# Optimization experiments

Measured on AMD Instinct MI355X. Metric: run time of the kernel, lower is better.

## Reference

```python
import jax, jax.numpy as jnp
import numpy as np

NUM_FEAT = 10
C_IN = 64


def setup_inputs() -> dict:
    key = jax.random.key(0)
    ks = jax.random.split(key, 8)
    B, T, C, H, W = 1, 8, C_IN, 32, 32
    scale = 1.0 / np.sqrt(C)
    return {
        "input1": jax.random.normal(ks[0], (B, T, C, H, W), dtype=jnp.float32),
        "input2": jax.random.normal(ks[1], (B, T, C, H, W), dtype=jnp.float32),
        "w1": jax.random.normal(ks[2], (NUM_FEAT, C), dtype=jnp.float32) * scale,
        "b1": jax.random.normal(ks[3], (NUM_FEAT,), dtype=jnp.float32) * scale,
        "w2": jax.random.normal(ks[4], (NUM_FEAT, C), dtype=jnp.float32) * scale,
        "b2": jax.random.normal(ks[5], (NUM_FEAT,), dtype=jnp.float32) * scale,
        "w3": jax.random.normal(ks[6], (NUM_FEAT, C), dtype=jnp.float32) * scale,
        "b3": jax.random.normal(ks[7], (NUM_FEAT,), dtype=jnp.float32) * scale,
    }


def reference(input1, input2, w1, b1, w2, b2, w3, b3):
    B, T, C, H, W = input1.shape
    N = T * H * W
    # transpose(1,2).reshape -> [B, C, T*H*W]
    x1 = input1.transpose(0, 2, 1, 3, 4).reshape(B, C, N)
    x2 = input2.transpose(0, 2, 1, 3, 4).reshape(B, C, N)
    # 1x1 Conv1d projections (act == 0 -> ReLU branch)
    q = jnp.einsum('fc,bcn->bnf', w1, x1) + b1            # [B, N, F]
    k = jnp.einsum('fc,bcn->bfn', w2, x2) + b2[:, None]   # [B, F, N]
    v = jnp.einsum('fc,bcn->bnf', w3, x1) + b3            # [B, N, F]
    scores = jax.nn.relu(jnp.einsum('bnf,bfm->bnm', q, k))  # [B, N, N]
    out = jnp.einsum('bnm,bmf->bnf', scores, v)             # [B, N, F]
    # view([B,T,H,W,F]).permute(0,1,4,2,3)
    return out.reshape(B, T, H, W, -1).transpose(0, 1, 4, 2, 3)
```

## Files before the change

kernel.cpp:

```cpp
#include <hip/hip_runtime.h>

typedef short  sv8 __attribute__((ext_vector_type(8)));
typedef float  fv16 __attribute__((ext_vector_type(16)));
typedef unsigned int uv4 __attribute__((ext_vector_type(4)));
typedef unsigned int uint32;
typedef unsigned short ushort16;

#define NF      10
#define CIN     64
#define NTOT    8192
#define HW      1024
#define FPAD    16
#define MSPLIT  16
#define MCHUNK  (NTOT / MSPLIT)
#define PSTRIDE 16

#define MFMA32(a, b, c) __builtin_amdgcn_mfma_f32_32x32x16_bf16((a), (b), (c), 0, 0, 0)

static __device__ inline ushort16 f32_to_bf16_rne(float x) {
    uint32 u = __builtin_bit_cast(uint32, x);
    u = (u + 0x7fffu + ((u >> 16) & 1u)) >> 16;
    return (ushort16)u;
}

__global__ __launch_bounds__(64) void qkv_kernel(
    const float* __restrict__ in1, const float* __restrict__ in2,
    const float* __restrict__ w1, const float* __restrict__ b1,
    const float* __restrict__ w2, const float* __restrict__ b2,
    const float* __restrict__ w3, const float* __restrict__ b3,
    ushort16* __restrict__ qb, ushort16* __restrict__ kb,
    ushort16* __restrict__ vfrag)
{
    __shared__ ushort16 lvs[64][FPAD];

    const int tid = threadIdx.x;
    const int n  = blockIdx.x * 64 + tid;
    const int t  = n >> 10;
    const int hw = n & 1023;

    if (blockIdx.y == 0) {
        const float* p = in1 + (size_t)t * (CIN * HW) + hw;
        float a[CIN];
#pragma unroll
        for (int c = 0; c < CIN; ++c) a[c] = p[c * HW];

        float aq[NF], av[NF];
#pragma unroll
        for (int f = 0; f < NF; ++f) { aq[f] = b1[f]; av[f] = b3[f]; }
#pragma unroll
        for (int c = 0; c < CIN; ++c) {
#pragma unroll
            for (int f = 0; f < NF; ++f) {
                aq[f] = fmaf(w1[f * CIN + c], a[c], aq[f]);
                av[f] = fmaf(w3[f * CIN + c], a[c], av[f]);
            }
        }
        ushort16 row[FPAD];
#pragma unroll
        for (int f = 0; f < NF; ++f) row[f] = f32_to_bf16_rne(aq[f]);
#pragma unroll
        for (int f = NF; f < FPAD; ++f) row[f] = 0;
        ushort16* dq = qb + (size_t)n * FPAD;
        ((uint4*)dq)[0] = ((const uint4*)row)[0];
        ((uint4*)dq)[1] = ((const uint4*)row)[1];

#pragma unroll
        for (int f = 0; f < NF; ++f) lvs[tid][f] = f32_to_bf16_rne(av[f]);
        __syncthreads();
        const int l  = tid & 31;
        const int tl = tid >> 5;
        char* base = (char*)vfrag + ((size_t)(blockIdx.x * 2 + tl)) * 2048;
#pragma unroll
        for (int fs = 0; fs < 2; ++fs) {
#pragma unroll
            for (int hh = 0; hh < 2; ++hh) {
                ushort16 buf[8];
#pragma unroll
                for (int j = 0; j < 8; ++j)
                    buf[j] = (l < NF) ? lvs[32 * tl + fs * 16 + 8 * hh + j][l]
                                      : (ushort16)0;
                *(uint4*)(base + fs * 1024 + (hh * 32 + l) * 16) =
                    *(const uint4*)buf;
            }
        }
    } else {
        const float* p = in2 + (size_t)t * (CIN * HW) + hw;
        float a[CIN];
#pragma unroll
        for (int c = 0; c < CIN; ++c) a[c] = p[c * HW];

        float ak[NF];
#pragma unroll
        for (int f = 0; f < NF; ++f) ak[f] = b2[f];
#pragma unroll
        for (int c = 0; c < CIN; ++c) {
#pragma unroll
            for (int f = 0; f < NF; ++f) ak[f] = fmaf(w2[f * CIN + c], a[c], ak[f]);
        }
        ushort16 row[FPAD];
#pragma unroll
        for (int f = 0; f < NF; ++f) row[f] = f32_to_bf16_rne(ak[f]);
#pragma unroll
        for (int f = NF; f < FPAD; ++f) row[f] = 0;
        ushort16* dk = kb + (size_t)n * FPAD;
        ((uint4*)dk)[0] = ((const uint4*)row)[0];
        ((uint4*)dk)[1] = ((const uint4*)row)[1];
    }
}

__global__ __launch_bounds__(256) void attn_mfma_kernel(
    const ushort16* __restrict__ qb, const ushort16* __restrict__ kb,
    const ushort16* __restrict__ vfrag, float* __restrict__ pws)
{
    const int lane = threadIdx.x & 63;
    const int wid  = threadIdx.x >> 6;
    const int col  = lane & 31;
    const int h    = lane >> 5;
    const int n0   = (blockIdx.x * 4 + wid) * 32;
    const int m0   = blockIdx.y * MCHUNK;

    const uint4 qraw = *(const uint4*)((const char*)qb + (size_t)(n0 + col) * 32 + h * 16);
    const sv8 qf = __builtin_bit_cast(sv8, qraw);

    const char* kbase = (const char*)kb + (size_t)(m0 + col) * 32 + h * 16;
    const char* vbase = (const char*)vfrag + (size_t)(m0 >> 5) * 2048 + lane * 16;

    fv16 zerov, acc1, acc2;
#pragma unroll
    for (int i = 0; i < 16; ++i) { zerov[i] = 0.f; acc1[i] = 0.f; acc2[i] = 0.f; }

    uint4 kf = *(const uint4*)kbase;
    uint4 v1 = *(const uint4*)vbase;
    uint4 v2 = *(const uint4*)(vbase + 1024);

    for (int s = 0; s < MCHUNK / 32; ++s) {
        uint4 kf_n = *(const uint4*)(kbase + (size_t)(s + 1) * 1024);
        uint4 v1_n = *(const uint4*)(vbase + (size_t)(s + 1) * 2048);
        uint4 v2_n = *(const uint4*)(vbase + (size_t)(s + 1) * 2048 + 1024);

        fv16 S = MFMA32(__builtin_bit_cast(sv8, kf), qf, zerov);

        uint32 p[8];
#pragma unroll
        for (int i = 0; i < 8; ++i) {
            float e0 = fmaxf(S[2 * i], 0.f);
            float e1 = fmaxf(S[2 * i + 1], 0.f);
            p[i] = __builtin_amdgcn_perm(__builtin_bit_cast(uint32, e1),
                                         __builtin_bit_cast(uint32, e0), 0x07060302u);
        }
        uint32 sw[8];
#pragma unroll
        for (int i = 0; i < 8; ++i)
            sw[i] = __shfl_xor((unsigned int)p[i], 32, 64);

        uv4 b1 = { h ? sw[2] : p[0], h ? sw[3] : p[1],
                   h ? p[2] : sw[0], h ? p[3] : sw[1] };
        uv4 b2 = { h ? sw[6] : p[4], h ? sw[7] : p[5],
                   h ? p[6] : sw[4], h ? p[7] : sw[5] };

        acc1 = MFMA32(__builtin_bit_cast(sv8, v1), __builtin_bit_cast(sv8, b1), acc1);
        acc2 = MFMA32(__builtin_bit_cast(sv8, v2), __builtin_bit_cast(sv8, b2), acc2);

        kf = kf_n; v1 = v1_n; v2 = v2_n;
    }

    const int n = n0 + col;
#pragma unroll
    for (int r = 0; r < 16; ++r) {
        int f = (r & 3) + 8 * (r >> 2) + 4 * h;
        if (f < NF)
            pws[((size_t)blockIdx.y * PSTRIDE + f) * NTOT + n] = acc1[r] + acc2[r];
    }
}

__global__ __launch_bounds__(256) void reduce_kernel(
    const float* __restrict__ pws, float* __restrict__ out)
{
    const int gid = blockIdx.x * 256 + threadIdx.x;
    const int f = gid >> 13;
    const int n = gid & (NTOT - 1);
    float s = 0.f;
#pragma unroll
    for (int y = 0; y < MSPLIT; ++y)
        s += pws[((size_t)y * PSTRIDE + f) * NTOT + n];
    const int t = n >> 10, hw = n & 1023;
    out[(size_t)t * (NF * HW) + f * HW + hw] = s;
}

extern "C" void kernel_launch(void* const* d_in, const int* in_sizes, int n_in,
                              void* d_out, int out_size, void* d_ws, size_t ws_size,
                              hipStream_t stream)
{
    const float* in1 = (const float*)d_in[0];
    const float* in2 = (const float*)d_in[1];
    const float* w1  = (const float*)d_in[2];
    const float* b1  = (const float*)d_in[3];
    const float* w2  = (const float*)d_in[4];
    const float* b2  = (const float*)d_in[5];
    const float* w3  = (const float*)d_in[6];
    const float* b3  = (const float*)d_in[7];

    ushort16* qb    = (ushort16*)d_ws;
    ushort16* kb    = qb + (size_t)NTOT * FPAD;
    ushort16* vfrag = kb + (size_t)NTOT * FPAD;
    float*    pws   = (float*)((char*)vfrag + 512 * 1024);
    float*    out   = (float*)d_out;

    qkv_kernel<<<dim3(NTOT / 64, 2), 64, 0, stream>>>(
        in1, in2, w1, b1, w2, b2, w3, b3, qb, kb, vfrag);

    attn_mfma_kernel<<<dim3(64, MSPLIT), 256, 0, stream>>>(qb, kb, vfrag, pws);

    reduce_kernel<<<dim3(NF * NTOT / 256), 256, 0, stream>>>(pws, out);
}
```

Measured before the change: 104.0 us.

## Fuse QKV, attention and reduction into one cooperative kernel with grid syncs

Merges the three kernels into a single cooperative launch of 512 blocks that use grid.sync() between the QKV projection, the MFMA attention and the split reduction. The aim is to remove two kernel launch gaps and the tail effects between stages. The key split drops from 16 to 8 so the attention stage fits 512 blocks, which gives fewer partial sums but half the parallelism per output column and longer per-wave loops. The QKV stage now runs on only 64 blocks while the others wait at the barrier, and grid syncs add their own cost.

```diff
diff --git a/kernel.cpp b/kernel.cpp
--- a/kernel.cpp
+++ b/kernel.cpp
@@ -1,4 +1,7 @@
 #include <hip/hip_runtime.h>
+#include <hip/hip_cooperative_groups.h>
+
+namespace cg = cooperative_groups;
 
 typedef short  sv8 __attribute__((ext_vector_type(8)));
 typedef float  fv16 __attribute__((ext_vector_type(16)));
@@ -11,7 +14,7 @@
 #define NTOT    8192
 #define HW      1024
 #define FPAD    16
-#define MSPLIT  16
+#define MSPLIT  8
 #define MCHUNK  (NTOT / MSPLIT)
 #define PSTRIDE 16
 
@@ -23,168 +26,181 @@
     return (ushort16)u;
 }
 
-__global__ __launch_bounds__(64) void qkv_kernel(
+__global__ __launch_bounds__(256, 2) void fused_kernel(
     const float* __restrict__ in1, const float* __restrict__ in2,
     const float* __restrict__ w1, const float* __restrict__ b1,
     const float* __restrict__ w2, const float* __restrict__ b2,
     const float* __restrict__ w3, const float* __restrict__ b3,
     ushort16* __restrict__ qb, ushort16* __restrict__ kb,
-    ushort16* __restrict__ vfrag)
+    ushort16* __restrict__ vfrag, float* __restrict__ pws,
+    float* __restrict__ out)
 {
-    __shared__ ushort16 lvs[64][FPAD];
-
-    const int tid = threadIdx.x;
-    const int n  = blockIdx.x * 64 + tid;
-    const int t  = n >> 10;
-    const int hw = n & 1023;
-
-    if (blockIdx.y == 0) {
-        const float* p = in1 + (size_t)t * (CIN * HW) + hw;
-        float a[CIN];
-#pragma unroll
-        for (int c = 0; c < CIN; ++c) a[c] = p[c * HW];
-
-        float aq[NF], av[NF];
-#pragma unroll
-        for (int f = 0; f < NF; ++f) { aq[f] = b1[f]; av[f] = b3[f]; }
-#pragma unroll
-        for (int c = 0; c < CIN; ++c) {
-#pragma unroll
-            for (int f = 0; f < NF; ++f) {
-                aq[f] = fmaf(w1[f * CIN + c], a[c], aq[f]);
-                av[f] = fmaf(w3[f * CIN + c], a[c], av[f]);
-            }
-        }
-        ushort16 row[FPAD];
-#pragma unroll
-        for (int f = 0; f < NF; ++f) row[f] = f32_to_bf16_rne(aq[f]);
-#pragma unroll
-        for (int f = NF; f < FPAD; ++f) row[f] = 0;
-        ushort16* dq = qb + (size_t)n * FPAD;
-        ((uint4*)dq)[0] = ((const uint4*)row)[0];
-        ((uint4*)dq)[1] = ((const uint4*)row)[1];
-
-#pragma unroll
-        for (int f = 0; f < NF; ++f) lvs[tid][f] = f32_to_bf16_rne(av[f]);
-        __syncthreads();
-        const int l  = tid & 31;
-        const int tl = tid >> 5;
-        char* base = (char*)vfrag + ((size_t)(blockIdx.x * 2 + tl)) * 2048;
-#pragma unroll
-        for (int fs = 0; fs < 2; ++fs) {
-#pragma unroll
-            for (int hh = 0; hh < 2; ++hh) {
-                ushort16 buf[8];
-#pragma unroll
-                for (int j = 0; j < 8; ++j)
-                    buf[j] = (l < NF) ? lvs[32 * tl + fs * 16 + 8 * hh + j][l]
-                                      : (ushort16)0;
-                *(uint4*)(base + fs * 1024 + (hh * 32 + l) * 16) =
-                    *(const uint4*)buf;
-            }
-        }
-    } else {
-        const float* p = in2 + (size_t)t * (CIN * HW) + hw;
-        float a[CIN];
-#pragma unroll
-        for (int c = 0; c < CIN; ++c) a[c] = p[c * HW];
-
-        float ak[NF];
-#pragma unroll
-        for (int f = 0; f < NF; ++f) ak[f] = b2[f];
-#pragma unroll
-        for (int c = 0; c < CIN; ++c) {
-#pragma unroll
-            for (int f = 0; f < NF; ++f) ak[f] = fmaf(w2[f * CIN + c], a[c], ak[f]);
-        }
-        ushort16 row[FPAD];
-#pragma unroll
-        for (int f = 0; f < NF; ++f) row[f] = f32_to_bf16_rne(ak[f]);
-#pragma unroll
-        for (int f = NF; f < FPAD; ++f) row[f] = 0;
-        ushort16* dk = kb + (size_t)n * FPAD;
-        ((uint4*)dk)[0] = ((const uint4*)row)[0];
-        ((uint4*)dk)[1] = ((const uint4*)row)[1];
+    cg::grid_group grid = cg::this_grid();
+
+    const int wid  = threadIdx.x >> 6;
+    const int lane = threadIdx.x & 63;
+
+    __shared__ ushort16 lvs[4][64][FPAD];
+
+    if (blockIdx.x < 64) {
+        const int wg   = blockIdx.x * 4 + wid;
+        const int side = wg >> 7;
+        const int g64  = wg & 127;
+        const int n    = g64 * 64 + lane;
+        const int t    = n >> 10;
+        const int hw   = n & 1023;
+
+        if (side == 0) {
+            const float* p = in1 + (size_t)t * (CIN * HW) + hw;
+            float aq[NF], av[NF];
+#pragma unroll
+            for (int f = 0; f < NF; ++f) { aq[f] = b1[f]; av[f] = b3[f]; }
+            for (int c0 = 0; c0 < CIN; c0 += 16) {
+                float a[16];
+#pragma unroll
+                for (int j = 0; j < 16; ++j) a[j] = p[(c0 + j) * HW];
+#pragma unroll
+                for (int j = 0; j < 16; ++j) {
+#pragma unroll
+                    for (int f = 0; f < NF; ++f) {
+                        aq[f] = fmaf(w1[f * CIN + c0 + j], a[j], aq[f]);
+                        av[f] = fmaf(w3[f * CIN + c0 + j], a[j], av[f]);
+                    }
+                }
+            }
+            ushort16 row[FPAD];
+#pragma unroll
+            for (int f = 0; f < NF; ++f) row[f] = f32_to_bf16_rne(aq[f]);
+#pragma unroll
+            for (int f = NF; f < FPAD; ++f) row[f] = 0;
+            ushort16* dq = qb + (size_t)n * FPAD;
+            ((uint4*)dq)[0] = ((const uint4*)row)[0];
+            ((uint4*)dq)[1] = ((const uint4*)row)[1];
+
+#pragma unroll
+            for (int f = 0; f < NF; ++f) lvs[wid][lane][f] = f32_to_bf16_rne(av[f]);
+            const int l  = lane & 31;
+            const int tl = lane >> 5;
+            char* base = (char*)vfrag + ((size_t)(g64 * 2 + tl)) * 2048;
+#pragma unroll
+            for (int fs = 0; fs < 2; ++fs) {
+#pragma unroll
+                for (int hh = 0; hh < 2; ++hh) {
+                    ushort16 buf[8];
+#pragma unroll
+                    for (int j = 0; j < 8; ++j)
+                        buf[j] = (l < NF) ? lvs[wid][32 * tl + fs * 16 + 8 * hh + j][l]
+                                          : (ushort16)0;
+                    *(uint4*)(base + fs * 1024 + (hh * 32 + l) * 16) =
+                        *(const uint4*)buf;
+                }
+            }
+        } else {
+            const float* p = in2 + (size_t)t * (CIN * HW) + hw;
+            float ak[NF];
+#pragma unroll
+            for (int f = 0; f < NF; ++f) ak[f] = b2[f];
+            for (int c0 = 0; c0 < CIN; c0 += 16) {
+                float a[16];
+#pragma unroll
+                for (int j = 0; j < 16; ++j) a[j] = p[(c0 + j) * HW];
+#pragma unroll
+                for (int j = 0; j < 16; ++j) {
+#pragma unroll
+                    for (int f = 0; f < NF; ++f)
+                        ak[f] = fmaf(w2[f * CIN + c0 + j], a[j], ak[f]);
+                }
+            }
+            ushort16 row[FPAD];
+#pragma unroll
+            for (int f = 0; f < NF; ++f) row[f] = f32_to_bf16_rne(ak[f]);
+#pragma unroll
+            for (int f = NF; f < FPAD; ++f) row[f] = 0;
+            ushort16* dk = kb + (size_t)n * FPAD;
+            ((uint4*)dk)[0] = ((const uint4*)row)[0];
+            ((uint4*)dk)[1] = ((const uint4*)row)[1];
+        }
     }
-}
-
-__global__ __launch_bounds__(256) void attn_mfma_kernel(
-    const ushort16* __restrict__ qb, const ushort16* __restrict__ kb,
-    const ushort16* __restrict__ vfrag, float* __restrict__ pws)
-{
-    const int lane = threadIdx.x & 63;
-    const int wid  = threadIdx.x >> 6;
-    const int col  = lane & 31;
-    const int h    = lane >> 5;
-    const int n0   = (blockIdx.x * 4 + wid) * 32;
-    const int m0   = blockIdx.y * MCHUNK;
-
-    const uint4 qraw = *(const uint4*)((const char*)qb + (size_t)(n0 + col) * 32 + h * 16);
-    const sv8 qf = __builtin_bit_cast(sv8, qraw);
-
-    const char* kbase = (const char*)kb + (size_t)(m0 + col) * 32 + h * 16;
-    const char* vbase = (const char*)vfrag + (size_t)(m0 >> 5) * 2048 + lane * 16;
-
-    fv16 zerov, acc1, acc2;
-#pragma unroll
-    for (int i = 0; i < 16; ++i) { zerov[i] = 0.f; acc1[i] = 0.f; acc2[i] = 0.f; }
-
-    uint4 kf = *(const uint4*)kbase;
-    uint4 v1 = *(const uint4*)vbase;
-    uint4 v2 = *(const uint4*)(vbase + 1024);
-
-    for (int s = 0; s < MCHUNK / 32; ++s) {
-        uint4 kf_n = *(const uint4*)(kbase + (size_t)(s + 1) * 1024);
-        uint4 v1_n = *(const uint4*)(vbase + (size_t)(s + 1) * 2048);
-        uint4 v2_n = *(const uint4*)(vbase + (size_t)(s + 1) * 2048 + 1024);
-
-        fv16 S = MFMA32(__builtin_bit_cast(sv8, kf), qf, zerov);
-
-        uint32 p[8];
-#pragma unroll
-        for (int i = 0; i < 8; ++i) {
-            float e0 = fmaxf(S[2 * i], 0.f);
-            float e1 = fmaxf(S[2 * i + 1], 0.f);
-            p[i] = __builtin_amdgcn_perm(__builtin_bit_cast(uint32, e1),
-                                         __builtin_bit_cast(uint32, e0), 0x07060302u);
-        }
-        uint32 sw[8];
-#pragma unroll
-        for (int i = 0; i < 8; ++i)
-            sw[i] = __shfl_xor((unsigned int)p[i], 32, 64);
-
-        uv4 b1 = { h ? sw[2] : p[0], h ? sw[3] : p[1],
-                   h ? p[2] : sw[0], h ? p[3] : sw[1] };
-        uv4 b2 = { h ? sw[6] : p[4], h ? sw[7] : p[5],
-                   h ? p[6] : sw[4], h ? p[7] : sw[5] };
-
-        acc1 = MFMA32(__builtin_bit_cast(sv8, v1), __builtin_bit_cast(sv8, b1), acc1);
-        acc2 = MFMA32(__builtin_bit_cast(sv8, v2), __builtin_bit_cast(sv8, b2), acc2);
-
-        kf = kf_n; v1 = v1_n; v2 = v2_n;
+
+    grid.sync();
+
+    {
+        const int bx  = blockIdx.x & 63;
+        const int by  = blockIdx.x >> 6;
+        const int col = lane & 31;
+        const int h   = lane >> 5;
+        const int n0  = (bx * 4 + wid) * 32;
+        const int m0  = by * MCHUNK;
+
+        const uint4 qraw = *(const uint4*)((const char*)qb + (size_t)(n0 + col) * 32 + h * 16);
+        const sv8 qf = __builtin_bit_cast(sv8, qraw);
+
+        const char* kbase = (const char*)kb + (size_t)(m0 + col) * 32 + h * 16;
+        const char* vbase = (const char*)vfrag + (size_t)(m0 >> 5) * 2048 + lane * 16;
+
+        fv16 zerov, acc1, acc2;
+#pragma unroll
+        for (int i = 0; i < 16; ++i) { zerov[i] = 0.f; acc1[i] = 0.f; acc2[i] = 0.f; }
+
+        uint4 kf = *(const uint4*)kbase;
+        uint4 v1 = *(const uint4*)vbase;
+        uint4 v2 = *(const uint4*)(vbase + 1024);
+
+        for (int s = 0; s < MCHUNK / 32; ++s) {
+            uint4 kf_n = *(const uint4*)(kbase + (size_t)(s + 1) * 1024);
+            uint4 v1_n = *(const uint4*)(vbase + (size_t)(s + 1) * 2048);
+            uint4 v2_n = *(const uint4*)(vbase + (size_t)(s + 1) * 2048 + 1024);
+
+            fv16 S = MFMA32(__builtin_bit_cast(sv8, kf), qf, zerov);
+
+            uint32 p[8];
+#pragma unroll
+            for (int i = 0; i < 8; ++i) {
+                float e0 = fmaxf(S[2 * i], 0.f);
+                float e1 = fmaxf(S[2 * i + 1], 0.f);
+                p[i] = __builtin_amdgcn_perm(__builtin_bit_cast(uint32, e1),
+                                             __builtin_bit_cast(uint32, e0), 0x07060302u);
+            }
+            uint32 sw[8];
+#pragma unroll
+            for (int i = 0; i < 8; ++i)
+                sw[i] = __shfl_xor((unsigned int)p[i], 32, 64);
+
+            uv4 b1 = { h ? sw[2] : p[0], h ? sw[3] : p[1],
+                       h ? p[2] : sw[0], h ? p[3] : sw[1] };
+            uv4 b2 = { h ? sw[6] : p[4], h ? sw[7] : p[5],
+                       h ? p[6] : sw[4], h ? p[7] : sw[5] };
+
+            acc1 = MFMA32(__builtin_bit_cast(sv8, v1), __builtin_bit_cast(sv8, b1), acc1);
+            acc2 = MFMA32(__builtin_bit_cast(sv8, v2), __builtin_bit_cast(sv8, b2), acc2);
+
+            kf = kf_n; v1 = v1_n; v2 = v2_n;
+        }
+
+        const int n = n0 + col;
+#pragma unroll
+        for (int r = 0; r < 16; ++r) {
+            int f = (r & 3) + 8 * (r >> 2) + 4 * h;
+            if (f < NF)
+                pws[((size_t)by * PSTRIDE + f) * NTOT + n] = acc1[r] + acc2[r];
+        }
     }
 
-    const int n = n0 + col;
-#pragma unroll
-    for (int r = 0; r < 16; ++r) {
-        int f = (r & 3) + 8 * (r >> 2) + 4 * h;
-        if (f < NF)
-            pws[((size_t)blockIdx.y * PSTRIDE + f) * NTOT + n] = acc1[r] + acc2[r];
+    grid.sync();
+
+    {
+        const int gid = blockIdx.x * 256 + threadIdx.x;
+        if (gid < NF * NTOT) {
+            const int f = gid >> 13;
+            const int n = gid & (NTOT - 1);
+            float s = 0.f;
+#pragma unroll
+            for (int y = 0; y < MSPLIT; ++y)
+                s += pws[((size_t)y * PSTRIDE + f) * NTOT + n];
+            const int t = n >> 10, hw = n & 1023;
+            out[(size_t)t * (NF * HW) + f * HW + hw] = s;
+        }
     }
-}
-
-__global__ __launch_bounds__(256) void reduce_kernel(
-    const float* __restrict__ pws, float* __restrict__ out)
-{
-    const int gid = blockIdx.x * 256 + threadIdx.x;
-    const int f = gid >> 13;
-    const int n = gid & (NTOT - 1);
-    float s = 0.f;
-#pragma unroll
-    for (int y = 0; y < MSPLIT; ++y)
-        s += pws[((size_t)y * PSTRIDE + f) * NTOT + n];
-    const int t = n >> 10, hw = n & 1023;
-    out[(size_t)t * (NF * HW) + f * HW + hw] = s;
 }
 
 extern "C" void kernel_launch(void* const* d_in, const int* in_sizes, int n_in,
@@ -206,10 +222,11 @@
     float*    pws   = (float*)((char*)vfrag + 512 * 1024);
     float*    out   = (float*)d_out;
 
-    qkv_kernel<<<dim3(NTOT / 64, 2), 64, 0, stream>>>(
-        in1, in2, w1, b1, w2, b2, w3, b3, qb, kb, vfrag);
-
-    attn_mfma_kernel<<<dim3(64, MSPLIT), 256, 0, stream>>>(qb, kb, vfrag, pws);
-
-    reduce_kernel<<<dim3(NF * NTOT / 256), 256, 0, stream>>>(pws, out);
+    void* args[] = {
+        (void*)&in1, (void*)&in2,
+        (void*)&w1, (void*)&b1, (void*)&w2, (void*)&b2, (void*)&w3, (void*)&b3,
+        (void*)&qb, (void*)&kb, (void*)&vfrag, (void*)&pws, (void*)&out
+    };
+    hipLaunchCooperativeKernel((const void*)fused_kernel,
+                               dim3(512), dim3(256), args, 0, stream);
 }
```

Result: slower. 220.9 us (+112.3%).
